# Kernel optimization log

Measured on AMD Instinct MI355X. Metric: run time of the kernel, lower is better.

Reference implementation:

```python
import jax, jax.numpy as jnp
import numpy as np

B, N, C, H, E = 4, 10000, 128, 128, 160000


def setup_inputs() -> dict:
    key = jax.random.key(0)
    ks = jax.random.split(key, 16)
    d_in = C + H
    s = 1.0 / np.sqrt(d_in)
    inp = {
        "x": jax.random.normal(ks[0], (B, N, C), jnp.float32),
        "h": jax.random.normal(ks[1], (B, N, H), jnp.float32),
        "c": jax.random.normal(ks[2], (B, N, H), jnp.float32),
        "edge_index": jax.random.randint(ks[3], (2, E), 0, N, jnp.int64),
        "edge_weight": jax.random.uniform(ks[4], (E,), jnp.float32),
        "W_i": jax.random.uniform(ks[5], (d_in, H), jnp.float32, -s, s),
        "b_i": jnp.zeros((H,), jnp.float32),
        "W_f": jax.random.uniform(ks[6], (d_in, H), jnp.float32, -s, s),
        "b_f": jnp.zeros((H,), jnp.float32),
        "W_o": jax.random.uniform(ks[7], (d_in, H), jnp.float32, -s, s),
        "b_o": jnp.zeros((H,), jnp.float32),
        "W_g": jax.random.uniform(ks[8], (d_in, H), jnp.float32, -s, s),
        "b_g": jnp.zeros((H,), jnp.float32),
    }
    return inp


def reference(x, h, c, edge_index, edge_weight, W_i, b_i, W_f, b_f, W_o, b_o, W_g, b_g):
    n = x.shape[1]
    hid = W_i.shape[1]
    src, dst = edge_index[0], edge_index[1]
    # GCNConv: add self-loops (weight 1.0) and symmetric normalization
    loop = jnp.arange(n)
    src_a = jnp.concatenate([src, loop])
    dst_a = jnp.concatenate([dst, loop])
    w_a = jnp.concatenate([edge_weight, jnp.ones((n,), edge_weight.dtype)])
    deg = jax.ops.segment_sum(w_a, dst_a, num_segments=n)  # [N]
    dinv = jnp.where(deg > 0, jax.lax.rsqrt(deg), 0.0)
    norm = dinv[src_a] * w_a * dinv[dst_a]  # [E+N]

    xh = jnp.concatenate([x, h], axis=-1)  # [B, N, C+H]
    # Fuse the four gate convs: same edge_index/normalization, shared gather-scatter
    W = jnp.concatenate([W_i, W_f, W_o, W_g], axis=1)  # [C+H, 4H]
    b = jnp.concatenate([b_i, b_f, b_o, b_g])  # [4H]
    xt = jnp.einsum("bnd,dh->bnh", xh, W)  # [B, N, 4H]
    msgs = xt[:, src_a, :] * norm[None, :, None]  # [B, E+N, 4H]
    agg = jnp.zeros_like(xt).at[:, dst_a, :].add(msgs) + b  # [B, N, 4H]

    i = jax.nn.sigmoid(agg[..., 0 * hid:1 * hid])
    f = jax.nn.sigmoid(agg[..., 1 * hid:2 * hid])
    o = jax.nn.sigmoid(agg[..., 2 * hid:3 * hid])
    g = jnp.tanh(agg[..., 3 * hid:4 * hid])
    c_new = f * c + i * g
    h_new = o * jnp.tanh(c_new)
    return h_new, c_new
```

## Files before the change

kernel.cpp:

```cpp
#include <hip/hip_runtime.h>
#include <math.h>

#define NB 4
#define NN 10000
#define NE 160000
#define DIN 256
#define DOUT 512
#define EPAD 310016

typedef _Float16 f16x8 __attribute__((ext_vector_type(8)));
typedef _Float16 f16x2 __attribute__((ext_vector_type(2)));
typedef float f32x4 __attribute__((ext_vector_type(4)));

struct hv4 { f16x2 p[4]; };

#define GLOAD_LDS16(g, l) \
    __builtin_amdgcn_global_load_lds((const __attribute__((address_space(1))) void*)(g), \
                                     (__attribute__((address_space(3))) void*)(l), 16, 0, 0)

__global__ __launch_bounds__(256) void k_packcvt(
        const float* __restrict__ Wi, const float* __restrict__ Wf,
        const float* __restrict__ Wo, const float* __restrict__ Wg,
        const float* __restrict__ bi, const float* __restrict__ bf,
        const float* __restrict__ bo, const float* __restrict__ bg,
        const int* __restrict__ ei, const float* __restrict__ ew,
        const float* __restrict__ x, const float* __restrict__ h,
        float* __restrict__ deg, int* __restrict__ cnt,
        _Float16* __restrict__ Wt2, float* __restrict__ bcat,
        _Float16* __restrict__ xhb) {
    int bid = blockIdx.x;
    int t = threadIdx.x;
    if (bid < 512) {
        int i = bid * 256 + t;
        int e = i & 7;
        int j = (i >> 3) & 127;
        int lk = (i >> 10) & 3;
        int kb = (i >> 12) & 7;
        int g = i >> 15;
        const float* W = (g == 0) ? Wi : (g == 1) ? Wf : (g == 2) ? Wo : Wg;
        Wt2[i] = (_Float16)W[(kb * 32 + lk * 8 + e) * 128 + j];
        if (i < DOUT) {
            int gg = i >> 7, jj = i & 127;
            const float* bb = (gg == 0) ? bi : (gg == 1) ? bf : (gg == 2) ? bo : bg;
            bcat[i] = bb[jj];
        }
    } else if (bid < 1137) {
        int e = (bid - 512) * 256 + t;
        int dst = ei[NE + e];
        atomicAdd(&deg[dst], ew[e]);
        atomicAdd(&cnt[dst], 1);
    } else {
        int id = (bid - 1137) * 256 + t;
        int f8 = id * 8;
        int row = f8 >> 8;
        int col = f8 & 255;
        int n = row >> 2, b = row & 3;
        const float* src = ((col >> 7) ? h : x) + ((size_t)b * NN + n) * 128 + (col & 127);
        float4 v0 = *(const float4*)src;
        float4 v1 = *(const float4*)(src + 4);
        f16x8 o;
        o[0] = (_Float16)v0.x; o[1] = (_Float16)v0.y;
        o[2] = (_Float16)v0.z; o[3] = (_Float16)v0.w;
        o[4] = (_Float16)v1.x; o[5] = (_Float16)v1.y;
        o[6] = (_Float16)v1.z; o[7] = (_Float16)v1.w;
        *(f16x8*)(xhb + (size_t)f8) = o;
    }
}

__global__ __launch_bounds__(1024) void k_scan(float* __restrict__ deg,
                                               const int* __restrict__ cnt,
                                               int* __restrict__ offsets) {
    int t = threadIdx.x;
    for (int i = t; i < NN; i += 1024) {
        deg[i] = rsqrtf(deg[i] + 1.0f);
    }
    __shared__ int wsum[16];
    int base = t * 10;
    int loc[10];
    int s = 0;
#pragma unroll
    for (int i = 0; i < 10; ++i) {
        int idx = base + i;
        int v = (idx < NN) ? ((cnt[idx] + 15) & ~15) : 0;
        loc[i] = s;
        s += v;
    }
    int lane = t & 63, w = t >> 6;
    int inc = s;
    for (int o = 1; o < 64; o <<= 1) {
        int u = __shfl_up(inc, o);
        if (lane >= o) inc += u;
    }
    if (lane == 63) wsum[w] = inc;
    __syncthreads();
    if (t < 16) {
        int v = wsum[t];
        for (int o = 1; o < 16; o <<= 1) {
            int u = __shfl_up(v, o);
            if (t >= o) v += u;
        }
        wsum[t] = v;
    }
    __syncthreads();
    int wave_excl = (w > 0) ? wsum[w - 1] : 0;
    int thread_excl = wave_excl + inc - s;
#pragma unroll
    for (int i = 0; i < 10; ++i) {
        int idx = base + i;
        if (idx < NN) offsets[idx] = thread_excl + loc[i];
    }
    if (t == 0) offsets[NN] = wsum[15];
}

__global__ __launch_bounds__(256) void k_fill(const int* __restrict__ ei,
                                              const float* __restrict__ ew,
                                              const float* __restrict__ dinv,
                                              const int* __restrict__ offsets,
                                              int* cursor, int2* __restrict__ ebuf) {
    int e = blockIdx.x * 256 + threadIdx.x;
    int src = ei[e], dst = ei[NE + e];
    float norm = dinv[src] * ew[e] * dinv[dst];
    unsigned short hw;
    {
        _Float16 hnorm = (_Float16)norm;
        hw = __builtin_bit_cast(unsigned short, hnorm);
    }
    int wpair = (int)hw | ((int)hw << 16);
    int pos = offsets[dst] + atomicAdd(&cursor[dst], 1);
    ebuf[pos] = make_int2(src * 2048, wpair);
}

__global__ __launch_bounds__(512) void k_agg(const _Float16* __restrict__ xhb,
                                             const float* __restrict__ dinv,
                                             const int* __restrict__ offsets,
                                             const int2* __restrict__ ebuf,
                                             _Float16* __restrict__ aggb) {
    int t = threadIdx.x;
    int lane = t & 63, wid = t >> 6;
    int bid = blockIdx.x;
    int xcd = bid & 7;
    int b = xcd >> 1, kh = xcd & 1;
    int n = (bid >> 3) * 8 + wid;
    int eg = lane >> 4;
    int fl16 = (lane & 15) << 4;

    const char* bb = (const char*)xhb + (b << 9) + (kh << 8);

    f16x2 pac0 = (f16x2)0, pac1 = (f16x2)0, pac2 = (f16x2)0, pac3 = (f16x2)0;

#define ACCH(E, V)                                          \
    {                                                       \
        f16x2 w2 = __builtin_bit_cast(f16x2, (E).y);        \
        pac0 = (V).p[0] * w2 + pac0;                        \
        pac1 = (V).p[1] * w2 + pac1;                        \
        pac2 = (V).p[2] * w2 + pac2;                        \
        pac3 = (V).p[3] * w2 + pac3;                        \
    }

    hv4 vS = *(const hv4*)(bb + n * 2048 + fl16);
    float di = dinv[n];

    int beg = offsets[n], end = offsets[n + 1];
    const char* ep = (const char*)ebuf + (size_t)beg * 8 + eg * 8;
    for (int j = beg; j < end; j += 16, ep += 128) {
        int2 e0 = *(const int2*)(ep);
        int2 e1 = *(const int2*)(ep + 32);
        int2 e2 = *(const int2*)(ep + 64);
        int2 e3 = *(const int2*)(ep + 96);
        hv4 v0 = *(const hv4*)(bb + e0.x + fl16);
        hv4 v1 = *(const hv4*)(bb + e1.x + fl16);
        hv4 v2 = *(const hv4*)(bb + e2.x + fl16);
        hv4 v3 = *(const hv4*)(bb + e3.x + fl16);
        ACCH(e0, v0);
        ACCH(e1, v1);
        ACCH(e2, v2);
        ACCH(e3, v3);
    }

    float a[8];
    a[0] = (float)pac0[0]; a[1] = (float)pac0[1];
    a[2] = (float)pac1[0]; a[3] = (float)pac1[1];
    a[4] = (float)pac2[0]; a[5] = (float)pac2[1];
    a[6] = (float)pac3[0]; a[7] = (float)pac3[1];
#pragma unroll
    for (int i = 0; i < 8; ++i) {
        a[i] += __shfl_xor(a[i], 16);
        a[i] += __shfl_xor(a[i], 32);
    }
    {
        float wl = di * di;
        a[0] = fmaf(wl, (float)vS.p[0][0], a[0]);
        a[1] = fmaf(wl, (float)vS.p[0][1], a[1]);
        a[2] = fmaf(wl, (float)vS.p[1][0], a[2]);
        a[3] = fmaf(wl, (float)vS.p[1][1], a[3]);
        a[4] = fmaf(wl, (float)vS.p[2][0], a[4]);
        a[5] = fmaf(wl, (float)vS.p[2][1], a[5]);
        a[6] = fmaf(wl, (float)vS.p[3][0], a[6]);
        a[7] = fmaf(wl, (float)vS.p[3][1], a[7]);
    }
    if (eg == 0) {
        f16x8 o;
#pragma unroll
        for (int i = 0; i < 8; ++i) o[i] = (_Float16)a[i];
        *(f16x8*)(aggb + ((size_t)b * NN + n) * 256 + (kh << 7) + (fl16 >> 1)) = o;
    }
}

__global__ __launch_bounds__(256, 2) void k_gemm(const _Float16* __restrict__ aggb,
                                                 const _Float16* __restrict__ Wt2,
                                                 const float* __restrict__ bcat,
                                                 const float* __restrict__ c_in,
                                                 float* __restrict__ out) {
    __shared__ __align__(16) _Float16 sA[64 * 256];
    int t = threadIdx.x;
    int lane = t & 63, wid = t >> 6;
    int lr = lane & 15, lk = lane >> 4;
    int bid = blockIdx.x;
    int rb = bid >> 1, jb = bid & 1;
    int rowbase = rb * 64;
    int jj = jb * 64 + wid * 16 + lr;

#pragma unroll
    for (int i = 0; i < 8; ++i) {
        int idx = i * 256 + t;
        int row = idx >> 5;
        int cb = (idx & 31) << 4;
        const char* g = (const char*)aggb + (size_t)(rowbase + row) * 512 + (cb ^ ((row & 7) << 4));
        char* l = (char*)sA + (size_t)(i * 256 + wid * 64) * 16;
        GLOAD_LDS16(g, l);
    }

    f16x8 breg[4][8];
#pragma unroll
    for (int g = 0; g < 4; ++g)
#pragma unroll
        for (int kb = 0; kb < 8; ++kb)
            breg[g][kb] = *(const f16x8*)(Wt2 + ((size_t)((g * 8 + kb) * 4 + lk) * 128 + jj) * 8);

    float b_i = bcat[jj], b_f = bcat[128 + jj], b_o = bcat[256 + jj], b_g = bcat[384 + jj];

    __syncthreads();

    f32x4 acc[4][4];
#pragma unroll
    for (int mi = 0; mi < 4; ++mi)
#pragma unroll
        for (int g = 0; g < 4; ++g) acc[mi][g] = (f32x4)0.f;

    int aswz = (lr & 7) << 4;
#pragma unroll
    for (int kb = 0; kb < 8; ++kb) {
        int koff = (kb << 6) + (lk << 4);
#pragma unroll
        for (int mi = 0; mi < 4; ++mi) {
            f16x8 a = *(const f16x8*)((const char*)sA + (mi * 16 + lr) * 512 + (koff ^ aswz));
            acc[mi][0] = __builtin_amdgcn_mfma_f32_16x16x32_f16(a, breg[0][kb], acc[mi][0], 0, 0, 0);
            acc[mi][1] = __builtin_amdgcn_mfma_f32_16x16x32_f16(a, breg[1][kb], acc[mi][1], 0, 0, 0);
            acc[mi][2] = __builtin_amdgcn_mfma_f32_16x16x32_f16(a, breg[2][kb], acc[mi][2], 0, 0, 0);
            acc[mi][3] = __builtin_amdgcn_mfma_f32_16x16x32_f16(a, breg[3][kb], acc[mi][3], 0, 0, 0);
        }
    }

#pragma unroll
    for (int mi = 0; mi < 4; ++mi) {
#pragma unroll
        for (int r = 0; r < 4; ++r) {
            int row = rowbase + mi * 16 + lk * 4 + r;
            size_t o = (size_t)row * 128 + jj;
            float vi = acc[mi][0][r] + b_i;
            float vf = acc[mi][1][r] + b_f;
            float vo = acc[mi][2][r] + b_o;
            float vg = acc[mi][3][r] + b_g;
            float ig = 1.f / (1.f + __expf(-vi));
            float fg = 1.f / (1.f + __expf(-vf));
            float og = 1.f / (1.f + __expf(-vo));
            float gg = 1.f - 2.f / (__expf(2.f * vg) + 1.f);
            float cn = fg * c_in[o] + ig * gg;
            float tc = 1.f - 2.f / (__expf(2.f * cn) + 1.f);
            out[o] = og * tc;
            out[(size_t)NB * NN * 128 + o] = cn;
        }
    }
}


extern "C" void kernel_launch(void* const* d_in, const int* in_sizes, int n_in,
                              void* d_out, int out_size, void* d_ws, size_t ws_size,
                              hipStream_t stream) {
    const float* x = (const float*)d_in[0];
    const float* h = (const float*)d_in[1];
    const float* c = (const float*)d_in[2];
    const int* ei = (const int*)d_in[3];
    const float* ew = (const float*)d_in[4];
    const float* Wi = (const float*)d_in[5];
    const float* bi = (const float*)d_in[6];
    const float* Wf = (const float*)d_in[7];
    const float* bf = (const float*)d_in[8];
    const float* Wo = (const float*)d_in[9];
    const float* bo = (const float*)d_in[10];
    const float* Wg = (const float*)d_in[11];
    const float* bg = (const float*)d_in[12];
    float* out = (float*)d_out;

    char* ws = (char*)d_ws;
    size_t off = 0;
    auto alloc = [&](size_t bytes) {
        void* p = ws + off;
        off = (off + bytes + 255) & ~(size_t)255;
        return p;
    };
    float* deg = (float*)alloc((size_t)NN * 4);
    int* cnt = (int*)alloc((size_t)NN * 4);
    int* cursor = (int*)alloc((size_t)NN * 4);
    int* offsets = (int*)alloc((size_t)(NN + 1) * 4);
    float* bcat = (float*)alloc((size_t)DOUT * 4);
    _Float16* Wt2 = (_Float16*)alloc((size_t)DOUT * DIN * 2);
    int2* ebuf = (int2*)alloc((size_t)EPAD * 8);
    _Float16* xhb = (_Float16*)alloc((size_t)NN * 4 * DIN * 2);
    _Float16* aggb = (_Float16*)alloc((size_t)NB * NN * DIN * 2);

    hipMemsetAsync(deg, 0, 3 * 40192, stream);
    hipMemsetAsync(ebuf, 0, (size_t)EPAD * 8, stream);

    hipLaunchKernelGGL(k_packcvt, dim3(6137), dim3(256), 0, stream,
                       Wi, Wf, Wo, Wg, bi, bf, bo, bg, ei, ew, x, h, deg, cnt, Wt2, bcat, xhb);
    hipLaunchKernelGGL(k_scan, dim3(1), dim3(1024), 0, stream, deg, cnt, offsets);
    hipLaunchKernelGGL(k_fill, dim3(625), dim3(256), 0, stream,
                       ei, ew, deg, offsets, cursor, ebuf);
    hipLaunchKernelGGL(k_agg, dim3(10000), dim3(512), 0, stream,
                       xhb, deg, offsets, ebuf, aggb);
    hipLaunchKernelGGL(k_gemm, dim3(1250), dim3(256), 0, stream,
                       aggb, Wt2, bcat, c, out);
}
```

Baseline: 125.6 us.

## Software-pipeline edge gathers in aggregation kernel and halve block size

The aggregation loop is restructured into a double-buffered software pipeline that prefetches the next group of 16 edges and their gathered feature rows while accumulating the current group. This hides gather latency behind FMA work. Blocks shrink from 8 to 4 nodes (256 threads, twice as many blocks), and the edge buffer padding grows so the one-group-ahead prefetch cannot read past the end. The cost is more live registers per thread, plus extra edge and feature loads at each node's tail that are fetched but never used.

```diff
diff --git a/kernel.cpp b/kernel.cpp
--- a/kernel.cpp
+++ b/kernel.cpp
@@ -6,7 +6,7 @@
 #define NE 160000
 #define DIN 256
 #define DOUT 512
-#define EPAD 310016
+#define EPAD 310080
 
 typedef _Float16 f16x8 __attribute__((ext_vector_type(8)));
 typedef _Float16 f16x2 __attribute__((ext_vector_type(2)));
@@ -130,7 +130,7 @@
     ebuf[pos] = make_int2(src * 2048, wpair);
 }
 
-__global__ __launch_bounds__(512) void k_agg(const _Float16* __restrict__ xhb,
+__global__ __launch_bounds__(256) void k_agg(const _Float16* __restrict__ xhb,
                                              const float* __restrict__ dinv,
                                              const int* __restrict__ offsets,
                                              const int2* __restrict__ ebuf,
@@ -140,11 +140,11 @@
     int bid = blockIdx.x;
     int xcd = bid & 7;
     int b = xcd >> 1, kh = xcd & 1;
-    int n = (bid >> 3) * 8 + wid;
+    int n = (bid >> 3) * 4 + wid;
     int eg = lane >> 4;
     int fl16 = (lane & 15) << 4;
 
-    const char* bb = (const char*)xhb + (b << 9) + (kh << 8);
+    const char* bbf = (const char*)xhb + (b << 9) + (kh << 8) + fl16;
 
     f16x2 pac0 = (f16x2)0, pac1 = (f16x2)0, pac2 = (f16x2)0, pac3 = (f16x2)0;
 
@@ -157,24 +157,45 @@
         pac3 = (V).p[3] * w2 + pac3;                        \
     }
 
-    hv4 vS = *(const hv4*)(bb + n * 2048 + fl16);
+    hv4 vS = *(const hv4*)(bbf + n * 2048);
     float di = dinv[n];
 
     int beg = offsets[n], end = offsets[n + 1];
+    int nw = (end - beg) >> 4;
     const char* ep = (const char*)ebuf + (size_t)beg * 8 + eg * 8;
-    for (int j = beg; j < end; j += 16, ep += 128) {
-        int2 e0 = *(const int2*)(ep);
-        int2 e1 = *(const int2*)(ep + 32);
-        int2 e2 = *(const int2*)(ep + 64);
-        int2 e3 = *(const int2*)(ep + 96);
-        hv4 v0 = *(const hv4*)(bb + e0.x + fl16);
-        hv4 v1 = *(const hv4*)(bb + e1.x + fl16);
-        hv4 v2 = *(const hv4*)(bb + e2.x + fl16);
-        hv4 v3 = *(const hv4*)(bb + e3.x + fl16);
-        ACCH(e0, v0);
-        ACCH(e1, v1);
-        ACCH(e2, v2);
-        ACCH(e3, v3);
+
+    int2 eA0 = *(const int2*)(ep);
+    int2 eA1 = *(const int2*)(ep + 32);
+    int2 eA2 = *(const int2*)(ep + 64);
+    int2 eA3 = *(const int2*)(ep + 96);
+    hv4 vA0 = *(const hv4*)(bbf + eA0.x);
+    hv4 vA1 = *(const hv4*)(bbf + eA1.x);
+    hv4 vA2 = *(const hv4*)(bbf + eA2.x);
+    hv4 vA3 = *(const hv4*)(bbf + eA3.x);
+
+    int w = 0;
+    for (; w + 2 <= nw; w += 2, ep += 256) {
+        int2 eB0 = *(const int2*)(ep + 128);
+        int2 eB1 = *(const int2*)(ep + 160);
+        int2 eB2 = *(const int2*)(ep + 192);
+        int2 eB3 = *(const int2*)(ep + 224);
+        hv4 vB0 = *(const hv4*)(bbf + eB0.x);
+        hv4 vB1 = *(const hv4*)(bbf + eB1.x);
+        hv4 vB2 = *(const hv4*)(bbf + eB2.x);
+        hv4 vB3 = *(const hv4*)(bbf + eB3.x);
+        ACCH(eA0, vA0); ACCH(eA1, vA1); ACCH(eA2, vA2); ACCH(eA3, vA3);
+        eA0 = *(const int2*)(ep + 256);
+        eA1 = *(const int2*)(ep + 288);
+        eA2 = *(const int2*)(ep + 320);
+        eA3 = *(const int2*)(ep + 352);
+        vA0 = *(const hv4*)(bbf + eA0.x);
+        vA1 = *(const hv4*)(bbf + eA1.x);
+        vA2 = *(const hv4*)(bbf + eA2.x);
+        vA3 = *(const hv4*)(bbf + eA3.x);
+        ACCH(eB0, vB0); ACCH(eB1, vB1); ACCH(eB2, vB2); ACCH(eB3, vB3);
+    }
+    if (w < nw) {
+        ACCH(eA0, vA0); ACCH(eA1, vA1); ACCH(eA2, vA2); ACCH(eA3, vA3);
     }
 
     float a[8];
@@ -327,7 +348,7 @@
     hipLaunchKernelGGL(k_scan, dim3(1), dim3(1024), 0, stream, deg, cnt, offsets);
     hipLaunchKernelGGL(k_fill, dim3(625), dim3(256), 0, stream,
                        ei, ew, deg, offsets, cursor, ebuf);
-    hipLaunchKernelGGL(k_agg, dim3(10000), dim3(512), 0, stream,
+    hipLaunchKernelGGL(k_agg, dim3(20000), dim3(256), 0, stream,
                        xhb, deg, offsets, ebuf, aggb);
     hipLaunchKernelGGL(k_gemm, dim3(1250), dim3(256), 0, stream,
                        aggb, Wt2, bcat, c, out);
```

New measurement: 131.9 us. 1.05x slower.
